# Kernel optimization log

Measured on AMD Instinct MI355X. Metric: run time of the kernel, lower is better.

## Reference

```python
import jax, jax.numpy as jnp
import numpy as np

B, L, D = 2, 2048, 1024
DH = 64
NH = D // DH
EPS = 1e-5
NEG = -1e30


def rms_norm(x, w):
    # x: (..., dh); norm in fp32 like the torch module, then scale by weight
    xf = x.astype(jnp.float32)
    y = xf * jax.lax.rsqrt(jnp.mean(xf * xf, axis=-1, keepdims=True) + EPS)
    return y.astype(x.dtype) * w.astype(x.dtype)


def sdpa(q, k, v, m):
    # q:(b,h,lq,dh) k,v:(b,h,lk,dh) m:(lq,lk) bool
    scale = 1.0 / jnp.sqrt(jnp.asarray(DH, q.dtype))
    s = jnp.einsum('bhqd,bhkd->bhqk', q, k) * scale
    s = jnp.where(m[None, None], s, NEG)
    p = jax.nn.softmax(s, axis=-1)
    return jnp.einsum('bhqk,bhkd->bhqd', p, v)


def setup_inputs() -> dict:
    key = jax.random.key(0)
    k1, k2, k3 = jax.random.split(key, 3)
    x = jax.random.normal(k1, (B, L, D), dtype=jnp.float32)
    mask = jnp.tril(jnp.ones((L, L), dtype=bool))  # causal: no fully-masked rows
    w_qkv = jax.random.normal(k2, (3 * D, D), dtype=jnp.float32) * (1.0 / np.sqrt(D))
    w_fc = jax.random.normal(k3, (D, D), dtype=jnp.float32) * (1.0 / np.sqrt(D))
    q_norm_w = jnp.ones((DH,), dtype=jnp.float32)
    k_norm_w = jnp.ones((DH,), dtype=jnp.float32)
    return {"x": x, "mask": mask, "w_qkv": w_qkv, "w_fc": w_fc,
            "q_norm_w": q_norm_w, "k_norm_w": k_norm_w,
            "subset_attention_size": 1024}


def reference(x, mask, w_qkv, w_fc, q_norm_w, k_norm_w, subset_attention_size):
    b, l, d = x.shape
    qkv = jnp.einsum('bld,ed->ble', x, w_qkv)  # (b,l,3d)
    q, k, v = jnp.split(qkv, 3, axis=-1)

    def heads(t):
        return t.reshape(b, l, NH, DH).transpose(0, 2, 1, 3)  # (b,nh,l,dh)

    q, k, v = heads(q), heads(k), heads(v)
    q = rms_norm(q, q_norm_w)
    k = rms_norm(k, k_norm_w)

    S = subset_attention_size
    if S is not None and S < l:
        o1 = sdpa(q[:, :, :S], k[:, :, :S], v[:, :, :S], mask[:S, :S])
        o2 = sdpa(q[:, :, S:], k, v, mask[S:, :])
        o = jnp.concatenate([o1, o2], axis=2)
    else:
        o = sdpa(q, k, v, mask)
    o = o.transpose(0, 2, 1, 3).reshape(b, l, d)  # (b,l,d)
    return jnp.einsum('bld,ed->ble', o, w_fc)
```

## Files before the change

### kernel.cpp

```cpp
#include <hip/hip_runtime.h>

typedef __bf16 bf16x8 __attribute__((ext_vector_type(8)));
typedef __bf16 bf16x4 __attribute__((ext_vector_type(4)));
typedef float f32x4 __attribute__((ext_vector_type(4)));
typedef short s16x4 __attribute__((ext_vector_type(4)));
typedef unsigned short u16;
typedef unsigned int u32;
typedef unsigned short u16x4 __attribute__((ext_vector_type(4)));
typedef unsigned short u16x8 __attribute__((ext_vector_type(8)));

#define AS1 __attribute__((address_space(1)))
#define AS3 __attribute__((address_space(3)))

__device__ __forceinline__ u16 f2bf(float f) {
  unsigned u = __builtin_bit_cast(unsigned, f);
  u += 0x7fffu + ((u >> 16) & 1u);
  return (u16)(u >> 16);
}

__device__ __forceinline__ float fast_exp2(float x) {
#if __has_builtin(__builtin_amdgcn_exp2f)
  return __builtin_amdgcn_exp2f(x);
#else
  return exp2f(x);
#endif
}

__device__ __forceinline__ f32x4 mfma16(s16x4 a, s16x4 b, f32x4 c) {
#if __has_builtin(__builtin_amdgcn_mfma_f32_16x16x16bf16_1k)
  return __builtin_amdgcn_mfma_f32_16x16x16bf16_1k(a, b, c, 0, 0, 0);
#else
  asm("v_mfma_f32_16x16x16_bf16 %0, %1, %2, %0" : "+v"(c) : "v"(a), "v"(b));
  return c;
#endif
}

__global__ __launch_bounds__(256) void cvt_all(const float* __restrict__ x,
                                               const float* __restrict__ wq,
                                               const float* __restrict__ wf,
                                               u16* __restrict__ xb, u16* __restrict__ wqb,
                                               u16* __restrict__ wfb) {
  long i = ((long)blockIdx.x * 256 + threadIdx.x) * 4;
  const float* src;
  u16* dst;
  long off;
  if (i < 4194304L) {
    src = x; dst = xb; off = i;
  } else if (i < 7340032L) {
    src = wq; dst = wqb; off = i - 4194304L;
  } else {
    src = wf; dst = wfb; off = i - 7340032L;
  }
  float4 v = *reinterpret_cast<const float4*>(src + off);
  u16x4 o;
  o.x = f2bf(v.x); o.y = f2bf(v.y); o.z = f2bf(v.z); o.w = f2bf(v.w);
  *reinterpret_cast<u16x4*>(dst + off) = o;
}

__global__ __launch_bounds__(256, 2) void gemm_qkv(const u16* __restrict__ A,
                                                   const u16* __restrict__ W,
                                                   u16* __restrict__ Qb,
                                                   u16* __restrict__ Kbf,
                                                   u16* __restrict__ vt,
                                                   const float* __restrict__ qw,
                                                   const float* __restrict__ kw) {
  constexpr int K = 1024;
  __shared__ __align__(16) u16 As[128 * 32];
  __shared__ __align__(16) u16 Bs[128 * 32];
  __shared__ __align__(16) u16 Ts[128 * 136];
  const int tid = threadIdx.x;
  const int lane = tid & 63;
  const int wid = tid >> 6;
  const int wm = wid >> 1, wn = wid & 1;
  const int l16 = lane & 15, g4 = lane >> 4;
  const long bm = blockIdx.x, bn = blockIdx.y;

  const int srow = tid >> 2;
  const int scol = (tid & 3) * 8;
  const u16* aA0 = A + (bm * 128 + srow) * (long)K + scol;
  const u16* aA1 = aA0 + 64 * (long)K;
  const u16* aW0 = W + (bn * 128 + srow) * (long)K + scol;
  const u16* aW1 = aW0 + 64 * (long)K;

  f32x4 acc[4][4] = {};

  for (int kt = 0; kt < K; kt += 32) {
    __builtin_amdgcn_global_load_lds((AS1 void*)(aA0 + kt), (AS3 void*)(&As[tid * 8]), 16, 0, 0);
    __builtin_amdgcn_global_load_lds((AS1 void*)(aA1 + kt), (AS3 void*)(&As[2048 + tid * 8]), 16, 0, 0);
    __builtin_amdgcn_global_load_lds((AS1 void*)(aW0 + kt), (AS3 void*)(&Bs[tid * 8]), 16, 0, 0);
    __builtin_amdgcn_global_load_lds((AS1 void*)(aW1 + kt), (AS3 void*)(&Bs[2048 + tid * 8]), 16, 0, 0);
    __syncthreads();
    bf16x8 af[4], bfr[4];
#pragma unroll
    for (int m = 0; m < 4; ++m)
      af[m] = *reinterpret_cast<const bf16x8*>(&As[(wm * 64 + m * 16 + l16) * 32 + g4 * 8]);
#pragma unroll
    for (int n = 0; n < 4; ++n)
      bfr[n] = *reinterpret_cast<const bf16x8*>(&Bs[(wn * 64 + n * 16 + l16) * 32 + g4 * 8]);
#pragma unroll
    for (int m = 0; m < 4; ++m)
#pragma unroll
      for (int n = 0; n < 4; ++n)
        acc[m][n] = __builtin_amdgcn_mfma_f32_16x16x32_bf16(af[m], bfr[n], acc[m][n], 0, 0, 0);
    __syncthreads();
  }

  if (bn < 16) {
    const float qscale = 0.18033688011112042f;
    const float* w = (bn < 8) ? qw : kw;
    const float ws = (bn < 8) ? qscale : 1.0f;
    float wv[4];
#pragma unroll
    for (int n = 0; n < 4; ++n) wv[n] = w[n * 16 + l16] * ws;
#pragma unroll
    for (int m = 0; m < 4; ++m) {
#pragma unroll
      for (int j = 0; j < 4; ++j) {
        float ss = 0.f;
#pragma unroll
        for (int n = 0; n < 4; ++n) ss = fmaf(acc[m][n][j], acc[m][n][j], ss);
        ss += __shfl_xor(ss, 1);
        ss += __shfl_xor(ss, 2);
        ss += __shfl_xor(ss, 4);
        ss += __shfl_xor(ss, 8);
        const float inv = rsqrtf(ss * (1.0f / 64.0f) + 1e-5f);
#pragma unroll
        for (int n = 0; n < 4; ++n) acc[m][n][j] *= inv * wv[n];
      }
    }
    u16* dst = (bn < 8) ? Qb : Kbf;
    const long cb = (bn < 8) ? bn : (bn - 8);
#pragma unroll
    for (int m = 0; m < 4; ++m)
#pragma unroll
      for (int n = 0; n < 4; ++n)
#pragma unroll
        for (int j = 0; j < 4; ++j) {
          long row = bm * 128 + wm * 64 + m * 16 + g4 * 4 + j;
          long col = cb * 128 + wn * 64 + n * 16 + l16;
          dst[row * 1024 + col] = f2bf(acc[m][n][j]);
        }
  } else {
#pragma unroll
    for (int m = 0; m < 4; ++m)
#pragma unroll
      for (int n = 0; n < 4; ++n) {
        bf16x4 w4;
#pragma unroll
        for (int j = 0; j < 4; ++j) w4[j] = (__bf16)acc[m][n][j];
        const int lc = wn * 64 + n * 16 + l16;
        const int lr = wm * 64 + m * 16 + g4 * 4;
        *reinterpret_cast<bf16x4*>(&Ts[lc * 136 + lr]) = w4;
      }
    __syncthreads();
    const int b = (int)(bm >> 4);
    const int keybase = ((int)(bm & 15)) * 128;
#pragma unroll
    for (int u = 0; u < 2; ++u) {
      const int unit = u * 256 + tid;
      const int hh = unit >> 8;
      const int d = (unit >> 2) & 63;
      const int kc = (unit & 3) * 32;
      const long bhv = b * 16 + (bn - 16) * 2 + hh;
      u16* dstp = vt + bhv * 131072L + (long)d * 2048 + keybase + kc;
      const u16* srcp = &Ts[(hh * 64 + d) * 136 + kc];
#pragma unroll
      for (int c = 0; c < 4; ++c)
        *reinterpret_cast<u16x8*>(dstp + c * 8) =
            *reinterpret_cast<const u16x8*>(srcp + c * 8);
    }
  }
}

__global__ __launch_bounds__(256, 2) void gemm_fc(const u16* __restrict__ A,
                                                  const u16* __restrict__ W,
                                                  float* __restrict__ C) {
  constexpr int N = 1024, K = 1024;
  __shared__ __align__(16) u16 As[128 * 32];
  __shared__ __align__(16) u16 Bs[64 * 32];
  const int tid = threadIdx.x;
  const int lane = tid & 63;
  const int wid = tid >> 6;
  const int wm = wid >> 1, wn = wid & 1;
  const int l16 = lane & 15, g4 = lane >> 4;
  const long bm = blockIdx.x, bn = blockIdx.y;

  const int srow = tid >> 2;
  const int scol = (tid & 3) * 8;
  const u16* aA0 = A + (bm * 128 + srow) * (long)K + scol;
  const u16* aA1 = aA0 + 64 * (long)K;
  const u16* aW0 = W + (bn * 64 + srow) * (long)K + scol;

  f32x4 acc[4][2] = {};

  for (int kt = 0; kt < K; kt += 32) {
    __builtin_amdgcn_global_load_lds((AS1 void*)(aA0 + kt), (AS3 void*)(&As[tid * 8]), 16, 0, 0);
    __builtin_amdgcn_global_load_lds((AS1 void*)(aA1 + kt), (AS3 void*)(&As[2048 + tid * 8]), 16, 0, 0);
    __builtin_amdgcn_global_load_lds((AS1 void*)(aW0 + kt), (AS3 void*)(&Bs[tid * 8]), 16, 0, 0);
    __syncthreads();
    bf16x8 af[4], bfr[2];
#pragma unroll
    for (int m = 0; m < 4; ++m)
      af[m] = *reinterpret_cast<const bf16x8*>(&As[(wm * 64 + m * 16 + l16) * 32 + g4 * 8]);
#pragma unroll
    for (int n = 0; n < 2; ++n)
      bfr[n] = *reinterpret_cast<const bf16x8*>(&Bs[(wn * 32 + n * 16 + l16) * 32 + g4 * 8]);
#pragma unroll
    for (int m = 0; m < 4; ++m)
#pragma unroll
      for (int n = 0; n < 2; ++n)
        acc[m][n] = __builtin_amdgcn_mfma_f32_16x16x32_bf16(af[m], bfr[n], acc[m][n], 0, 0, 0);
    __syncthreads();
  }

#pragma unroll
  for (int m = 0; m < 4; ++m)
#pragma unroll
    for (int n = 0; n < 2; ++n)
#pragma unroll
      for (int j = 0; j < 4; ++j) {
        long row = bm * 128 + wm * 64 + m * 16 + g4 * 4 + j;
        long col = bn * 64 + wn * 32 + n * 16 + l16;
        C[row * N + col] = acc[m][n][j];
      }
}

__global__ __launch_bounds__(256, 4) void attn_causal(const u16* __restrict__ Qb,
                                                      const u16* __restrict__ Kbf,
                                                      const u16* __restrict__ vt,
                                                      u16* __restrict__ o) {
  __shared__ __align__(16) u16 SMEM[16384];

  const int tid = threadIdx.x, lane = tid & 63, wid = tid >> 6;
  const int l16 = lane & 15, g4 = lane >> 4;
  const int h8 = (l16 & 7) << 4;
  const int qh = wid & 1, kh = wid >> 1;

  const int f = blockIdx.x;
  const int xcd = f & 7;
  const int g = f >> 3;
  const int hb = g >> 5;
  const int w = g & 31;
  const int bh = xcd * 4 + hb;
  const int basei = (w & 1) ? (31 - (w >> 1)) : (w >> 1);
  const int it = (hb & 1) ? (31 - basei) : basei;

  const long base = (long)(bh >> 4) * 2048 * 1024 + (bh & 15) * 64;
  const u16* qb = Qb + base;
  const u16* kb = Kbf + base;
  const u16* vtb = vt + (long)bh * 131072;

  bf16x8 qv[2][2];
#pragma unroll
  for (int qf = 0; qf < 2; ++qf) {
    const u16* qp = qb + ((long)it * 64 + qh * 32 + qf * 16 + l16) * 1024;
    qv[qf][0] = *reinterpret_cast<const bf16x8*>(qp + g4 * 8);
    qv[qf][1] = *reinterpret_cast<const bf16x8*>(qp + 32 + g4 * 8);
  }

  f32x4 acc[2][4] = {};
  f32x4 lacc[2] = {};

  s16x4 ones4;
#pragma unroll
  for (int j = 0; j < 4; ++j) ones4[j] = (short)0x3F80;

  const int krow = tid >> 3;
  const int scolE = (((tid & 7) * 16) ^ ((krow & 7) << 4)) >> 1;

  auto stage_issue = [&](int buf, int kt) {
    u16* KB = SMEM + buf * 4096;
    u16* VB = SMEM + 8192 + buf * 4096;
    __builtin_amdgcn_global_load_lds((AS1 void*)(kb + (long)(kt * 64 + krow) * 1024 + scolE),
                                     (AS3 void*)(&KB[tid * 8]), 16, 0, 0);
    __builtin_amdgcn_global_load_lds((AS1 void*)(kb + (long)(kt * 64 + krow + 32) * 1024 + scolE),
                                     (AS3 void*)(&KB[2048 + tid * 8]), 16, 0, 0);
    __builtin_amdgcn_global_load_lds((AS1 void*)(vtb + (long)krow * 2048 + kt * 64 + scolE),
                                     (AS3 void*)(&VB[tid * 8]), 16, 0, 0);
    __builtin_amdgcn_global_load_lds((AS1 void*)(vtb + (long)(krow + 32) * 2048 + kt * 64 + scolE),
                                     (AS3 void*)(&VB[2048 + tid * 8]), 16, 0, 0);
  };

  auto tile_step = [&](int cur, bool diag) {
    if (diag && qh == 0 && kh == 1) return;
    const u16* KB = SMEM + cur * 4096;
    const u16* VB = SMEM + 8192 + cur * 4096;
    bf16x8 kfr[2][2];
#pragma unroll
    for (int kf = 0; kf < 2; ++kf) {
      const int row = kh * 32 + kf * 16 + l16;
#pragma unroll
      for (int ck = 0; ck < 2; ++ck)
        kfr[kf][ck] = *reinterpret_cast<const bf16x8*>(
            &KB[row * 64 + (((ck * 64 + g4 * 16) ^ h8) >> 1)]);
    }
    f32x4 s[2][2];
    __builtin_amdgcn_s_setprio(1);
#pragma unroll
    for (int kf = 0; kf < 2; ++kf)
#pragma unroll
      for (int qf = 0; qf < 2; ++qf) {
        f32x4 z = {0.f, 0.f, 0.f, 0.f};
        z = __builtin_amdgcn_mfma_f32_16x16x32_bf16(kfr[kf][0], qv[qf][0], z, 0, 0, 0);
        z = __builtin_amdgcn_mfma_f32_16x16x32_bf16(kfr[kf][1], qv[qf][1], z, 0, 0, 0);
        s[kf][qf] = z;
      }
    __builtin_amdgcn_s_setprio(0);
    if (diag) {
#pragma unroll
      for (int kf = 0; kf < 2; ++kf)
#pragma unroll
        for (int qf = 0; qf < 2; ++qf) {
          const int keyl = kh * 32 + kf * 16 + g4 * 4;
          const int ql = qh * 32 + qf * 16 + l16;
#pragma unroll
          for (int j = 0; j < 4; ++j)
            if (keyl + j > ql) s[kf][qf][j] = -3e38f;
        }
    }
    s16x4 pfr[2][2];
#pragma unroll
    for (int kf = 0; kf < 2; ++kf)
#pragma unroll
      for (int qf = 0; qf < 2; ++qf) {
        bf16x4 p;
#pragma unroll
        for (int j = 0; j < 4; ++j) p[j] = (__bf16)fast_exp2(s[kf][qf][j]);
        pfr[kf][qf] = __builtin_bit_cast(s16x4, p);
      }
    __builtin_amdgcn_s_setprio(1);
#pragma unroll
    for (int qf = 0; qf < 2; ++qf) {
      lacc[qf] = mfma16(pfr[0][qf], ones4, lacc[qf]);
      lacc[qf] = mfma16(pfr[1][qf], ones4, lacc[qf]);
    }
#pragma unroll
    for (int db = 0; db < 4; ++db) {
      const int vrow = db * 16 + l16;
#pragma unroll
      for (int kf = 0; kf < 2; ++kf) {
        const u16x4 vv = *reinterpret_cast<const u16x4*>(
            &VB[vrow * 64 + (((kh * 64 + kf * 32 + g4 * 8) ^ h8) >> 1)]);
        const s16x4 vf = __builtin_bit_cast(s16x4, vv);
#pragma unroll
        for (int qf = 0; qf < 2; ++qf) acc[qf][db] = mfma16(pfr[kf][qf], vf, acc[qf][db]);
      }
    }
    __builtin_amdgcn_s_setprio(0);
  };

  stage_issue(0, 0);
  __syncthreads();

  for (int kt = 0; kt < it; ++kt) {
    const int cur = kt & 1;
    stage_issue(cur ^ 1, kt + 1);
    tile_step(cur, false);
    __syncthreads();
  }
  tile_step(it & 1, true);
  __syncthreads();

  float* Ebuf = reinterpret_cast<float*>(SMEM);
  const int ebase = qh * 2176;
  if (kh == 1) {
#pragma unroll
    for (int qf = 0; qf < 2; ++qf) {
#pragma unroll
      for (int db = 0; db < 4; ++db)
#pragma unroll
        for (int j = 0; j < 4; ++j)
          Ebuf[ebase + (qf * 16 + g4 * 4 + j) * 68 + db * 16 + l16] = acc[qf][db][j];
      if (l16 == 0) {
#pragma unroll
        for (int j = 0; j < 4; ++j)
          Ebuf[ebase + (qf * 16 + g4 * 4 + j) * 68 + 64] = lacc[qf][j];
      }
    }
  }
  __syncthreads();
  if (kh == 0) {
    const long obase = (long)(bh >> 4) * 2048 * 1024 + (bh & 15) * 64;
#pragma unroll
    for (int qf = 0; qf < 2; ++qf) {
      float linv[4];
#pragma unroll
      for (int j = 0; j < 4; ++j) {
        const float lsum = lacc[qf][j] + Ebuf[ebase + (qf * 16 + g4 * 4 + j) * 68 + 64];
        linv[j] = 1.0f / lsum;
      }
#pragma unroll
      for (int db = 0; db < 4; ++db)
#pragma unroll
        for (int j = 0; j < 4; ++j) {
          const int row = qh * 32 + qf * 16 + g4 * 4 + j;
          const float v =
              acc[qf][db][j] + Ebuf[ebase + (qf * 16 + g4 * 4 + j) * 68 + db * 16 + l16];
          o[obase + ((long)it * 64 + row) * 1024 + db * 16 + l16] = f2bf(v * linv[j]);
        }
    }
  }
}

extern "C" void kernel_launch(void* const* d_in, const int* in_sizes, int n_in,
                              void* d_out, int out_size, void* d_ws, size_t ws_size,
                              hipStream_t stream) {
  const float* x = (const float*)d_in[0];
  const float* w_qkv = (const float*)d_in[2];
  const float* w_fc = (const float*)d_in[3];
  const float* qw = (const float*)d_in[4];
  const float* kw = (const float*)d_in[5];
  float* out = (float*)d_out;

  char* ws = (char*)d_ws;
  u16* xb    = (u16*)(ws);
  u16* wqkvb = (u16*)(ws + (8L << 20));
  u16* wfcb  = (u16*)(ws + (14L << 20));
  u16* Qb    = (u16*)(ws + (16L << 20));
  u16* Kbf   = (u16*)(ws + (24L << 20));
  u16* vt    = (u16*)(ws + (32L << 20));
  u16* ob    = (u16*)(ws + (40L << 20));

  cvt_all<<<8192, 256, 0, stream>>>(x, w_qkv, w_fc, xb, wqkvb, wfcb);
  gemm_qkv<<<dim3(32, 24), 256, 0, stream>>>(xb, wqkvb, Qb, Kbf, vt, qw, kw);
  attn_causal<<<1024, 256, 0, stream>>>(Qb, Kbf, vt, ob);
  gemm_fc<<<dim3(32, 16), 256, 0, stream>>>(ob, wfcb, out);
}
```

Measured before the change: 98.12 us.

## Double-buffer LDS tiles in QKV and FC GEMM main loops

Both GEMM kernels now use two LDS buffers per operand. The next K-slice's global-to-LDS loads are issued before the MFMA work on the current slice, so memory latency can overlap compute and one barrier per iteration is dropped. In the QKV kernel the transpose scratch buffer is aliased onto the A/B staging area, which keeps total LDS no larger than before despite the doubled buffers. This depends on the remaining end-of-iteration barrier, and the wait it implies, to order the prefetch against reads of the other buffer.

```diff
diff --git a/kernel.cpp b/kernel.cpp
--- a/kernel.cpp
+++ b/kernel.cpp
@@ -65,9 +65,11 @@
                                                    const float* __restrict__ qw,
                                                    const float* __restrict__ kw) {
   constexpr int K = 1024;
-  __shared__ __align__(16) u16 As[128 * 32];
-  __shared__ __align__(16) u16 Bs[128 * 32];
-  __shared__ __align__(16) u16 Ts[128 * 136];
+  __shared__ __align__(16) u16 SMEM[17408];
+  u16* As = SMEM;
+  u16* Bs = SMEM + 8192;
+  u16* Ts = SMEM;
+
   const int tid = threadIdx.x;
   const int lane = tid & 63;
   const int wid = tid >> 6;
@@ -84,19 +86,32 @@
 
   f32x4 acc[4][4] = {};
 
-  for (int kt = 0; kt < K; kt += 32) {
-    __builtin_amdgcn_global_load_lds((AS1 void*)(aA0 + kt), (AS3 void*)(&As[tid * 8]), 16, 0, 0);
-    __builtin_amdgcn_global_load_lds((AS1 void*)(aA1 + kt), (AS3 void*)(&As[2048 + tid * 8]), 16, 0, 0);
-    __builtin_amdgcn_global_load_lds((AS1 void*)(aW0 + kt), (AS3 void*)(&Bs[tid * 8]), 16, 0, 0);
-    __builtin_amdgcn_global_load_lds((AS1 void*)(aW1 + kt), (AS3 void*)(&Bs[2048 + tid * 8]), 16, 0, 0);
-    __syncthreads();
+  auto stage = [&](int buf, int kt) {
+    __builtin_amdgcn_global_load_lds((AS1 void*)(aA0 + kt),
+                                     (AS3 void*)(&As[buf * 4096 + tid * 8]), 16, 0, 0);
+    __builtin_amdgcn_global_load_lds((AS1 void*)(aA1 + kt),
+                                     (AS3 void*)(&As[buf * 4096 + 2048 + tid * 8]), 16, 0, 0);
+    __builtin_amdgcn_global_load_lds((AS1 void*)(aW0 + kt),
+                                     (AS3 void*)(&Bs[buf * 4096 + tid * 8]), 16, 0, 0);
+    __builtin_amdgcn_global_load_lds((AS1 void*)(aW1 + kt),
+                                     (AS3 void*)(&Bs[buf * 4096 + 2048 + tid * 8]), 16, 0, 0);
+  };
+
+  stage(0, 0);
+  __syncthreads();
+
+  for (int t = 0; t < K / 32; ++t) {
+    const int cur = t & 1;
+    if (t + 1 < K / 32) stage(cur ^ 1, (t + 1) * 32);
     bf16x8 af[4], bfr[4];
 #pragma unroll
     for (int m = 0; m < 4; ++m)
-      af[m] = *reinterpret_cast<const bf16x8*>(&As[(wm * 64 + m * 16 + l16) * 32 + g4 * 8]);
+      af[m] = *reinterpret_cast<const bf16x8*>(
+          &As[cur * 4096 + (wm * 64 + m * 16 + l16) * 32 + g4 * 8]);
 #pragma unroll
     for (int n = 0; n < 4; ++n)
-      bfr[n] = *reinterpret_cast<const bf16x8*>(&Bs[(wn * 64 + n * 16 + l16) * 32 + g4 * 8]);
+      bfr[n] = *reinterpret_cast<const bf16x8*>(
+          &Bs[cur * 4096 + (wn * 64 + n * 16 + l16) * 32 + g4 * 8]);
 #pragma unroll
     for (int m = 0; m < 4; ++m)
 #pragma unroll
@@ -176,8 +191,8 @@
                                                   const u16* __restrict__ W,
                                                   float* __restrict__ C) {
   constexpr int N = 1024, K = 1024;
-  __shared__ __align__(16) u16 As[128 * 32];
-  __shared__ __align__(16) u16 Bs[64 * 32];
+  __shared__ __align__(16) u16 As[2][128 * 32];
+  __shared__ __align__(16) u16 Bs[2][64 * 32];
   const int tid = threadIdx.x;
   const int lane = tid & 63;
   const int wid = tid >> 6;
@@ -193,18 +208,25 @@
 
   f32x4 acc[4][2] = {};
 
-  for (int kt = 0; kt < K; kt += 32) {
-    __builtin_amdgcn_global_load_lds((AS1 void*)(aA0 + kt), (AS3 void*)(&As[tid * 8]), 16, 0, 0);
-    __builtin_amdgcn_global_load_lds((AS1 void*)(aA1 + kt), (AS3 void*)(&As[2048 + tid * 8]), 16, 0, 0);
-    __builtin_amdgcn_global_load_lds((AS1 void*)(aW0 + kt), (AS3 void*)(&Bs[tid * 8]), 16, 0, 0);
-    __syncthreads();
+  auto stage = [&](int buf, int kt) {
+    __builtin_amdgcn_global_load_lds((AS1 void*)(aA0 + kt), (AS3 void*)(&As[buf][tid * 8]), 16, 0, 0);
+    __builtin_amdgcn_global_load_lds((AS1 void*)(aA1 + kt), (AS3 void*)(&As[buf][2048 + tid * 8]), 16, 0, 0);
+    __builtin_amdgcn_global_load_lds((AS1 void*)(aW0 + kt), (AS3 void*)(&Bs[buf][tid * 8]), 16, 0, 0);
+  };
+
+  stage(0, 0);
+  __syncthreads();
+
+  for (int t = 0; t < K / 32; ++t) {
+    const int cur = t & 1;
+    if (t + 1 < K / 32) stage(cur ^ 1, (t + 1) * 32);
     bf16x8 af[4], bfr[2];
 #pragma unroll
     for (int m = 0; m < 4; ++m)
-      af[m] = *reinterpret_cast<const bf16x8*>(&As[(wm * 64 + m * 16 + l16) * 32 + g4 * 8]);
+      af[m] = *reinterpret_cast<const bf16x8*>(&As[cur][(wm * 64 + m * 16 + l16) * 32 + g4 * 8]);
 #pragma unroll
     for (int n = 0; n < 2; ++n)
-      bfr[n] = *reinterpret_cast<const bf16x8*>(&Bs[(wn * 32 + n * 16 + l16) * 32 + g4 * 8]);
+      bfr[n] = *reinterpret_cast<const bf16x8*>(&Bs[cur][(wn * 32 + n * 16 + l16) * 32 + g4 * 8]);
 #pragma unroll
     for (int m = 0; m < 4; ++m)
 #pragma unroll
```

New measurement: 103.1 us. 1.05x slower.
